# Optimization experiments

Measured on AMD Instinct MI355X. Metric: run time of the kernel, lower is better.

The kernel has to match this reference:

```python
import jax, jax.numpy as jnp
import numpy as np

V = 78864; E = 300; H = 512; A = 300; T = 20; DEC_EMB = 512; START = 2


def _pos_encoding(n, d):
    pos = np.arange(n)[:, None].astype(np.float32)
    i = np.arange(d)[None, :]
    angle = pos / np.power(10000.0, (2 * (i // 2)).astype(np.float32) / d)
    pe = np.where(i % 2 == 0, np.sin(angle), np.cos(angle)).astype(np.float32)
    return jnp.asarray(pe)  # [n, d]


def _lstm_cell(x, h, c, Wih, Whh, b):
    g = x @ Wih.T + h @ Whh.T + b
    i, f, gg, o = jnp.split(g, 4, axis=-1)
    c = jax.nn.sigmoid(f) * c + jax.nn.sigmoid(i) * jnp.tanh(gg)
    h = jax.nn.sigmoid(o) * jnp.tanh(c)
    return h, c


def setup_inputs() -> dict:
    key = jax.random.key(0)
    ks = iter(jax.random.split(key, 48))
    B, L = 40, 1000
    def w(shape, s=0.02):
        return jax.random.normal(next(ks), shape, jnp.float32) * s
    def z(shape):
        return jnp.zeros(shape, jnp.float32)
    inp = dict(
        enc_in=jax.random.randint(next(ks), (B, L), 0, V),
        enc_out=jax.random.normal(next(ks), (B, L, H), jnp.float32),
        enc_mask=jnp.zeros((B, L), bool),
        inputs=jax.random.randint(next(ks), (B, T), 0, V),
        embed=w((V, E)),
        elmo1_Wih=w((4 * H, E)), elmo1_Whh=w((4 * H, H)), elmo1_b=z((4 * H,)),
        elmo2_Wih=w((4 * H, H)), elmo2_Whh=w((4 * H, H)), elmo2_b=z((4 * H,)),
        in_W=w((DEC_EMB, H + E + A + H)), in_b=z((DEC_EMB,)),
        rnn1_Wih=w((4 * H, DEC_EMB)), rnn1_Whh=w((4 * H, H)), rnn1_b=z((4 * H,)),
        att1_Wq=w((A, H)), att1_bq=z((A,)), att1_Wk=w((A, H)), att1_bk=z((A,)), att1_Wv=w((A, H)), att1_bv=z((A,)),
        rnn2_Wih=w((4 * H, A)), rnn2_Whh=w((4 * H, H)), rnn2_b=z((4 * H,)),
        att2_Wq=w((A, H)), att2_bq=z((A,)), att2_Wk=w((A, H)), att2_bk=z((A,)), att2_Wv=w((A, H)), att2_bv=z((A,)),
        copy_W=w((A, H)), copy_b=z((A,)),
        out_W=w((V, A)), out_b=z((V,)),
        scale=jnp.asarray(1.0, jnp.float32),
    )
    return inp


def _forward(enc_in, enc_out, enc_mask, inputs, embed,
             elmo1_Wih, elmo1_Whh, elmo1_b, elmo2_Wih, elmo2_Whh, elmo2_b,
             in_W, in_b, rnn1_Wih, rnn1_Whh, rnn1_b,
             att1_Wq, att1_bq, att1_Wk, att1_bk, att1_Wv, att1_bv,
             rnn2_Wih, rnn2_Whh, rnn2_b,
             att2_Wq, att2_bq, att2_Wk, att2_bk, att2_Wv, att2_bv,
             copy_W, copy_b, out_W, out_b, scale):
    B, L = enc_in.shape
    pe = _pos_encoding(T, DEC_EMB)  # [T, 512]
    # Precompute per-encoder projections (hoisted out of the step loop).
    K1 = jnp.einsum('blh,ah->bla', enc_out, att1_Wk) + att1_bk
    V1 = jnp.einsum('blh,ah->bla', enc_out, att1_Wv) + att1_bv
    K2 = jnp.einsum('blh,ah->bla', enc_out, att2_Wk) + att2_bk
    V2 = jnp.einsum('blh,ah->bla', enc_out, att2_Wv) + att2_bv
    copyK = jnp.tanh(jnp.einsum('blh,ah->bla', enc_out, copy_W) + copy_b)
    bidx = jnp.arange(B)[:, None]

    def attn(h, Wq, bq, K, Vp):
        q = h @ Wq.T + bq                          # [B, A]
        s = jnp.einsum('ba,bla->bl', q, K)
        s = jnp.where(enc_mask, -1e9, s)
        p = jax.nn.softmax(s, axis=-1)
        return jnp.einsum('bl,bla->ba', p, Vp)

    # teacher forcing with random_int=0 -> always use ground-truth inputs
    sym_in = jnp.concatenate([jnp.full((B, 1), START, inputs.dtype), inputs[:, :-1]], axis=1).T  # [T,B]
    sym_out = inputs.T  # [T,B]

    zf = lambda *s: jnp.zeros(s, enc_out.dtype)
    carry0 = (zf(B, H), zf(B, H), zf(B, H), zf(B, H),  # elmo h1,c1,h2,c2
              zf(B, H), zf(B, H), zf(B, H), zf(B, H),  # rnn1 h,c ; rnn2 h,c
              zf(B, A), zf(B, H))                       # dec_att_out, select_read

    def step(carry, xs):
        eh1, ec1, eh2, ec2, h1, c1, h2, c2, att, sel = carry
        pe_t, s_in, s_out = xs
        emb = embed[s_in]                                           # [B, E]
        eh1, ec1 = _lstm_cell(emb, eh1, ec1, elmo1_Wih, elmo1_Whh, elmo1_b)
        eh2, ec2 = _lstm_cell(eh1, eh2, ec2, elmo2_Wih, elmo2_Whh, elmo2_b)
        in_embed = jnp.concatenate([emb, eh2], axis=-1)              # [B, 812]
        dec_in = jnp.concatenate([in_embed, att, sel], axis=-1) @ in_W.T + in_b + pe_t
        h1, c1 = _lstm_cell(dec_in, h1, c1, rnn1_Wih, rnn1_Whh, rnn1_b)
        att = attn(h1, att1_Wq, att1_bq, K1, V1)
        h2, c2 = _lstm_cell(att, h2, c2, rnn2_Wih, rnn2_Whh, rnn2_b)
        att = attn(h2, att2_Wq, att2_bq, K2, V2) + att
        # copy scores
        s = jnp.einsum('ba,bla->bl', att, copyK)
        s = jnp.where(enc_mask, -1e9, s)
        score_c = jax.nn.softmax(s, axis=-1)
        score_e = score_c * scale * scale
        vocab = att @ out_W.T + out_b                                # [B, V]
        vocab = vocab.at[bidx, enc_in].add(score_e)
        sym_pred = jnp.argmax(vocab, axis=-1).astype(jnp.int32)
        eq = (enc_in == s_out[:, None]).astype(score_c.dtype)
        score_f = score_c * eq
        score_f = score_f / (jnp.sum(score_f, axis=-1, keepdims=True) + 1e-8)
        sel = jnp.einsum('bl,blh->bh', score_f, enc_out)
        return (eh1, ec1, eh2, ec2, h1, c1, h2, c2, att, sel), (vocab, sym_pred)

    _, (dec_out, syms) = jax.lax.scan(step, carry0, (pe, sym_in, sym_out))
    return jnp.transpose(dec_out, (1, 0, 2)), syms.T  # [B,T,V], [B,T]


def reference(enc_in, enc_out, enc_mask, inputs, embed,
              elmo1_Wih, elmo1_Whh, elmo1_b, elmo2_Wih, elmo2_Whh, elmo2_b,
              in_W, in_b, rnn1_Wih, rnn1_Whh, rnn1_b,
              att1_Wq, att1_bq, att1_Wk, att1_bk, att1_Wv, att1_bv,
              rnn2_Wih, rnn2_Whh, rnn2_b,
              att2_Wq, att2_bq, att2_Wk, att2_bk, att2_Wv, att2_bv,
              copy_W, copy_b, out_W, out_b, scale):
    return _forward(enc_in, enc_out, enc_mask, inputs, embed,
                    elmo1_Wih, elmo1_Whh, elmo1_b, elmo2_Wih, elmo2_Whh, elmo2_b,
                    in_W, in_b, rnn1_Wih, rnn1_Whh, rnn1_b,
                    att1_Wq, att1_bq, att1_Wk, att1_bk, att1_Wv, att1_bv,
                    rnn2_Wih, rnn2_Whh, rnn2_b,
                    att2_Wq, att2_bq, att2_Wk, att2_bk, att2_Wv, att2_bv,
                    copy_W, copy_b, out_W, out_b, scale)
```

## Files before the change

kernel.cpp:

```cpp
#include <hip/hip_runtime.h>
#include <math.h>

#define B_ 40
#define L_ 1000
#define H_ 512
#define A_ 300
#define T_ 20
#define E_ 300
#define V_ 78864
#define START_ 2

#define NBLK 256
#define NTHR 512
#define NVT 309

#define OFF_CKH   0ul
#define OFF_M1T   6400000ul
#define OFF_M2T   6662144ul
#define OFF_BQK1  6924288ul
#define OFF_BQK2  6924800ul
#define OFF_QK    6925312ul
#define OFF_DEC   6945792ul
#define OFF_ATT1  6966272ul
#define OFF_CPART 6978272ul
#define OFF_CSTAT 7101152ul
#define OFF_ATTA  7101632ul
#define OFF_SCCA  7341632ul
#define OFF_STT   8141632ul
#define OFF_ATT2  8469312ul
#define OFF_SELP  8481312ul
#define OFF_FLAGS 8604192ul
#define OFF_REL   8612384ul
#define WS_END    8612448ul

struct P {
  const int* enc_in; const float* enc; const unsigned char* mask; const int* inputs;
  const float* embed;
  const float *e1Wih,*e1Whh,*e1b,*e2Wih,*e2Whh,*e2b;
  const float *inW,*inb;
  const float *r1Wih,*r1Whh,*r1b;
  const float *a1Wq,*a1bq,*a1Wk,*a1Wv,*a1bv;
  const float *r2Wih,*r2Whh,*r2b;
  const float *a2Wq,*a2bq,*a2Wk,*a2Wv,*a2bv;
  const float *cW,*cb,*oW,*ob,*scale;
  float* dout;
  unsigned short* copyKh;
  float *M1T,*M2T,*bqk1,*bqk2,*qk,*dec,*att1,*cpart,*cstat,*attTall,*sccAll,*stt,*att2,*selp;
  unsigned *flags,*rel;
};

__device__ __forceinline__ float sigm(float x){ return 1.0f/(1.0f+expf(-x)); }

__device__ __forceinline__ float wredSum(float v){
#pragma unroll
  for(int o=32;o>0;o>>=1) v+=__shfl_xor(v,o);
  return v;
}
__device__ __forceinline__ float wredMax(float v){
#pragma unroll
  for(int o=32;o>0;o>>=1) v=fmaxf(v,__shfl_xor(v,o));
  return v;
}
__device__ __forceinline__ unsigned short f2bf(float f){
  unsigned u=__float_as_uint(f);
  u=(u+0x7fffu+((u>>16)&1u))>>16;
  return (unsigned short)u;
}

__device__ __forceinline__ void gbar2(unsigned* flags, unsigned* rel, unsigned epoch){
  __syncthreads();
  int tid=threadIdx.x;
  if(blockIdx.x==0){
    if(tid>0 && tid<NBLK){
      while(__hip_atomic_load(flags+(unsigned)tid*32u,__ATOMIC_RELAXED,__HIP_MEMORY_SCOPE_AGENT)<epoch)
        __builtin_amdgcn_s_sleep(2);
      (void)__hip_atomic_load(flags+(unsigned)tid*32u,__ATOMIC_ACQUIRE,__HIP_MEMORY_SCOPE_AGENT);
    }
    __syncthreads();
    if(tid==0)
      __hip_atomic_store(rel,epoch,__ATOMIC_RELEASE,__HIP_MEMORY_SCOPE_AGENT);
  } else {
    if(tid==0){
      __hip_atomic_store(flags+(unsigned)blockIdx.x*32u,epoch,__ATOMIC_RELEASE,__HIP_MEMORY_SCOPE_AGENT);
      while(__hip_atomic_load(rel,__ATOMIC_RELAXED,__HIP_MEMORY_SCOPE_AGENT)<epoch)
        __builtin_amdgcn_s_sleep(2);
      (void)__hip_atomic_load(rel,__ATOMIC_ACQUIRE,__HIP_MEMORY_SCOPE_AGENT);
    }
    __syncthreads();
  }
}

template<typename SRC>
static __device__ __forceinline__ void gv_accum(float* xs,int K,const float* Wrow,
    float& acc,int lane,int kq,int nq,SRC src){
  for(int k0=0;k0<K;k0+=256){
    int ch=min(256,K-k0);
    __syncthreads();
    if(ch==256){
      float r[20];
#pragma unroll
      for(int u=0;u<20;u++){
        int i=threadIdx.x+u*NTHR;
        r[u]=src(i>>8,k0+(i&255));
      }
#pragma unroll
      for(int u=0;u<20;u++){
        int i=threadIdx.x+u*NTHR;
        xs[(i>>8)*257+(i&255)]=r[u];
      }
    } else {
      for(int i=threadIdx.x;i<40*ch;i+=NTHR){
        int bb=i/ch, kk=i-bb*ch;
        xs[bb*257+kk]=src(bb,k0+kk);
      }
    }
    __syncthreads();
    if(lane<40){
      float a0=0.f,a1=0.f,a2=0.f,a3=0.f;
      int k=kq;
      for(;k+3*nq<ch;k+=4*nq){
        a0+=Wrow[k0+k     ]*xs[lane*257+k];
        a1+=Wrow[k0+k+  nq]*xs[lane*257+k+  nq];
        a2+=Wrow[k0+k+2*nq]*xs[lane*257+k+2*nq];
        a3+=Wrow[k0+k+3*nq]*xs[lane*257+k+3*nq];
      }
      for(;k<ch;k+=nq) a0+=Wrow[k0+k]*xs[lane*257+k];
      acc+=a0+a1+a2+a3;
    }
  }
}

static __device__ void lstm_ph(const P& p,float* SH,float* gld,int t,
    const float* Wih,int XD,const float* Whh,const float* bias,
    const float* xvec,bool gather,
    const float* hr,const float* cr,float* hw,float* cw){
  int tid=threadIdx.x,w=tid>>6,lane=tid&63;
  int gate=w&3,usub=w>>2;
  int row=gate*H_+(blockIdx.x*2+usub);
  int rowu=__builtin_amdgcn_readfirstlane(row);
  float acc=bias[rowu];
  const float* W1=Wih+(size_t)rowu*XD;
  if(gather){
    const int* inp=p.inputs; const float* emb=p.embed; int tt=t;
    gv_accum(SH,XD,W1,acc,lane,0,1,[=](int bb,int kk)->float{
      int si=(tt==0)?START_:inp[bb*T_+tt-1];
      return emb[(size_t)si*E_+kk];});
  }else{
    gv_accum(SH,XD,W1,acc,lane,0,1,[=](int bb,int kk)->float{
      return xvec[(size_t)bb*XD+kk];});
  }
  const float* W2=Whh+(size_t)rowu*H_;
  gv_accum(SH,H_,W2,acc,lane,0,1,[=](int bb,int kk)->float{
    return hr[bb*H_+kk];});
  gld[w*64+lane]=acc;
  __syncthreads();
  if(w<2&&lane<40){
    int u=blockIdx.x*2+w,b=lane;
    float gi=gld[(w*4+0)*64+b],gf=gld[(w*4+1)*64+b],gg=gld[(w*4+2)*64+b],go=gld[(w*4+3)*64+b];
    float c=cr[b*H_+u];
    float cn=sigm(gf)*c+sigm(gi)*tanhf(gg);
    hw[b*H_+u]=sigm(go)*tanhf(cn);
    cw[b*H_+u]=cn;
  }
  __syncthreads();
}

static __device__ void qk_ph(const P& p,float* SH,const float* hsrc,
    const float* MT,const float* bqk){
  int tid=threadIdx.x;
  if(blockIdx.x>=240) return;
  int b=blockIdx.x/6, j=blockIdx.x%6;
  SH[tid]=hsrc[b*H_+tid];
  __syncthreads();
  int h0=j*86, hc=min(86,H_-h0);
  if(tid<hc){
    int hp=h0+tid;
    float a=bqk[hp];
    const float4* mr=(const float4*)(MT+(size_t)hp*H_);
#pragma unroll 8
    for(int i=0;i<H_/4;i++){
      float4 m4=mr[i];
      a+=SH[4*i]*m4.x+SH[4*i+1]*m4.y+SH[4*i+2]*m4.z+SH[4*i+3]*m4.w;
    }
    p.qk[b*H_+hp]=a;
  }
}

static __device__ void scctx_ph(const P& p,float* SH){
  int tid=threadIdx.x,w=tid>>6,lane=tid&63;
  if(blockIdx.x>=240) return;
  int b=blockIdx.x/6, j=blockIdx.x%6;
  int l0=j*167, lcnt=min(167,L_-l0);
  const float* qrow=p.qk+b*H_;
  float4 q0=*(const float4*)(qrow+lane*8);
  float4 q1=*(const float4*)(qrow+lane*8+4);
  float* tile=SH;
  float* sc24=SH+12288;
  const float4* base=(const float4*)(p.enc+((size_t)(b*L_+l0))*H_);
  float4 pre[6];
  { int rem=lcnt*128;
#pragma unroll
    for(int u=0;u<6;u++){ int i=tid+u*NTHR; pre[u]=(i<rem)?base[i]:make_float4(0.f,0.f,0.f,0.f); } }
  float m=-3.0e38f,S=0.f,acc=0.f;
  for(int t0=0;t0<lcnt;t0+=24){
    int tc=min(24,lcnt-t0);
    __syncthreads();
    { float4* dst=(float4*)tile;
#pragma unroll
      for(int u=0;u<6;u++){ int i=tid+u*NTHR; if(i<tc*128) dst[i]=pre[u]; } }
    __syncthreads();
    if(t0+24<lcnt){
      int rem=(lcnt-t0-24)*128;
      const float4* src=base+(size_t)(t0+24)*128;
#pragma unroll
      for(int u=0;u<6;u++){ int i=tid+u*NTHR; pre[u]=(i<rem)?src[i]:make_float4(0.f,0.f,0.f,0.f); }
    }
#pragma unroll
    for(int r=0;r<3;r++){
      int row=w*3+r;
      float sc=-1e30f;
      if(row<tc){
        const float4* er=(const float4*)(tile+row*512);
        float4 e0=er[lane*2], e1=er[lane*2+1];
        float pp=q0.x*e0.x+q0.y*e0.y+q0.z*e0.z+q0.w*e0.w
                +q1.x*e1.x+q1.y*e1.y+q1.z*e1.z+q1.w*e1.w;
        pp=wredSum(pp);
        sc=p.mask[b*L_+l0+t0+row]?-1e9f:pp;
      }
      if(lane==0) sc24[row]=sc;
    }
    __syncthreads();
    float tm=-3.0e38f;
    for(int r=0;r<tc;r++) tm=fmaxf(tm,sc24[r]);
    float mn=fmaxf(m,tm);
    float scl=expf(m-mn);
    float Sadd=0.f, aadd=0.f;
    for(int r=0;r<tc;r++){
      float pe=expf(sc24[r]-mn);
      Sadd+=pe;
      aadd+=pe*tile[r*512+tid];
    }
    S=S*scl+Sadd;
    acc=acc*scl+aadd;
    m=mn;
  }
  p.cpart[(size_t)(b*6+j)*H_+tid]=acc;
  if(tid==0){p.cstat[(b*6+j)*2]=m; p.cstat[(b*6+j)*2+1]=S;}
}

static __device__ void atto_ph(const P& p,float* SH,const float* Wv,const float* bv,
    bool ADD,int t){
  int tid=threadIdx.x;
  if(blockIdx.x>=40) return;
  int b=blockIdx.x;
  float mb=-3.0e38f;
#pragma unroll
  for(int j=0;j<6;j++) mb=fmaxf(mb,p.cstat[(b*6+j)*2]);
  float Sb=0.f;
#pragma unroll
  for(int j=0;j<6;j++) Sb+=p.cstat[(b*6+j)*2+1]*expf(p.cstat[(b*6+j)*2]-mb);
  float inv=1.0f/Sb;
  float cx=0.f;
#pragma unroll
  for(int j=0;j<6;j++) cx+=expf(p.cstat[(b*6+j)*2]-mb)*p.cpart[(size_t)(b*6+j)*H_+tid];
  SH[tid]=cx*inv;
  __syncthreads();
  if(tid<A_){
    float a=bv[tid];
    const float4* wr=(const float4*)(Wv+(size_t)tid*H_);
#pragma unroll 8
    for(int i=0;i<H_/4;i++){
      float4 w4=wr[i];
      a+=SH[4*i]*w4.x+SH[4*i+1]*w4.y+SH[4*i+2]*w4.z+SH[4*i+3]*w4.w;
    }
    if(ADD){
      a+=p.att1[b*A_+tid];
      p.att2[b*A_+tid]=a;
      p.attTall[(size_t)t*A_*B_+tid*B_+b]=a;
    }
    else p.att1[b*A_+tid]=a;
  }
}

static __device__ void copysc_ph(const P& p,int t){
  int tid=threadIdx.x,w=tid>>6,lane=tid&63;
  if(blockIdx.x>=240) return;
  int b=blockIdx.x/6, j=blockIdx.x%6;
  int l0=j*167, lcnt=min(167,L_-l0);
  float* scct=p.sccAll+(size_t)t*B_*L_;
  float ar[8];
#pragma unroll
  for(int q=0;q<8;q++){
    int a=lane*8+q;
    ar[q]=(lane<40&&a<A_)? p.att2[b*A_+a] : 0.f;
  }
  for(int l=l0+w;l<l0+lcnt;l+=8){
    float pp=0.f;
    if(lane<40){
      const uint4* cr=(const uint4*)(p.copyKh+((size_t)(b*L_+l))*320);
      uint4 kk=cr[lane];
      pp =ar[0]*__uint_as_float(kk.x<<16)+ar[1]*__uint_as_float(kk.x&0xffff0000u);
      pp+=ar[2]*__uint_as_float(kk.y<<16)+ar[3]*__uint_as_float(kk.y&0xffff0000u);
      pp+=ar[4]*__uint_as_float(kk.z<<16)+ar[5]*__uint_as_float(kk.z&0xffff0000u);
      pp+=ar[6]*__uint_as_float(kk.w<<16)+ar[7]*__uint_as_float(kk.w&0xffff0000u);
    }
    pp=wredSum(pp);
    if(lane==0) scct[b*L_+l]=p.mask[b*L_+l]?-1e9f:pp;
  }
}

static __device__ void sel_ph(const P& p,float* SH,float* red,int t){
  int tid=threadIdx.x,w=tid>>6,lane=tid&63;
  if(blockIdx.x>=240) return;
  int b=blockIdx.x/6, j=blockIdx.x%6;
  int l0=j*167, lcnt=min(167,L_-l0);
  const float* scct=p.sccAll+(size_t)t*B_*L_;
  for(int i=tid;i<L_;i+=NTHR) SH[i]=scct[b*L_+i];
  __syncthreads();
  float lm=-3.0e38f;
  for(int i=tid;i<L_;i+=NTHR) lm=fmaxf(lm,SH[i]);
  lm=wredMax(lm);
  if(lane==0) red[w]=lm;
  __syncthreads();
  float m=red[0];
#pragma unroll
  for(int q=1;q<8;q++) m=fmaxf(m,red[q]);
  __syncthreads();
  int so=p.inputs[b*T_+t];
  float ls=0.f,lq=0.f;
  for(int i=tid;i<L_;i+=NTHR){
    float exv=expf(SH[i]-m);
    ls+=exv;
    if(p.enc_in[b*L_+i]==so) lq+=exv;
  }
  ls=wredSum(ls); lq=wredSum(lq);
  if(lane==0){red[w]=ls; red[8+w]=lq;}
  __syncthreads();
  float S=0.f,Q=0.f;
#pragma unroll
  for(int q=0;q<8;q++){S+=red[q];Q+=red[8+q];}
  if(tid<lcnt){
    int l=l0+tid;
    float exv=expf(SH[l]-m);
    SH[1024+tid]=(p.enc_in[b*L_+l]==so)?exv:0.f;
  }
  __syncthreads();
  int h4=tid&127, rg=tid>>7;
  float4 a4=make_float4(0.f,0.f,0.f,0.f);
#pragma unroll 2
  for(int li=rg;li<lcnt;li+=4){
    float wgt=SH[1024+li];
    float4 ev=*(const float4*)(p.enc+((size_t)(b*L_+l0+li))*H_+h4*4);
    a4.x+=wgt*ev.x; a4.y+=wgt*ev.y; a4.z+=wgt*ev.z; a4.w+=wgt*ev.w;
  }
  *(float4*)(SH+2048+tid*4)=a4;
  __syncthreads();
  float inv=1.0f/(Q+1e-8f*S);
  float s=SH[2048+tid]+SH[2048+512+tid]+SH[2048+1024+tid]+SH[2048+1536+tid];
  p.selp[(size_t)(b*6+j)*H_+tid]=s*inv;
}

__global__ __launch_bounds__(NTHR,2) void k_persist(P p){
  __shared__ float SH[12544];
  __shared__ float gld[512];
  __shared__ float red[16];
  int blk=blockIdx.x, tid=threadIdx.x;
  unsigned bt=0;
#define BARR() do{bt++; gbar2(p.flags,p.rel,bt);}while(0)

  {
    int mm=blk>>7, r0=(blk&127)*4;
    const float* Wq = mm? p.a2Wq : p.a1Wq;
    const float* Wk = mm? p.a2Wk : p.a1Wk;
    float* MT = mm? p.M2T : p.M1T;
    float s0=0.f,s1=0.f,s2=0.f,s3=0.f;
    for(int a=0;a<A_;a++){
      float wq=Wq[a*H_+tid];
      s0+=wq*Wk[a*H_+r0+0];
      s1+=wq*Wk[a*H_+r0+1];
      s2+=wq*Wk[a*H_+r0+2];
      s3+=wq*Wk[a*H_+r0+3];
    }
    MT[(size_t)(r0+0)*H_+tid]=s0;
    MT[(size_t)(r0+1)*H_+tid]=s1;
    MT[(size_t)(r0+2)*H_+tid]=s2;
    MT[(size_t)(r0+3)*H_+tid]=s3;
    if((blk&127)==0){
      const float* bq = mm? p.a2bq : p.a1bq;
      float ab=0.f;
      for(int a=0;a<A_;a++) ab+=bq[a]*Wk[a*H_+tid];
      (mm? p.bqk2 : p.bqk1)[tid]=ab;
    }
  }
  for(int item=blk;item<B_*63;item+=NBLK){
    int b=item/63, lt=item-b*63;
    int l0=lt*16, lcnt=min(16,L_-l0);
    float acc[16];
    float bv=(tid<A_)?p.cb[tid]:0.f;
#pragma unroll
    for(int l=0;l<16;l++) acc[l]=bv;
    for(int k0=0;k0<H_;k0+=32){
      __syncthreads();
      for(int i=tid;i<A_*32;i+=NTHR){
        int a=i>>5,kc=i&31;
        SH[a*33+kc]=p.cW[(size_t)a*H_+k0+kc];
      }
      __syncthreads();
      if(tid<A_){
#pragma unroll
        for(int l=0;l<16;l++){
          if(l<lcnt){
            const float* es=p.enc+((size_t)(b*L_+l0+l))*H_+k0;
            float al=acc[l];
#pragma unroll
            for(int kc=0;kc<32;kc++) al+=SH[tid*33+kc]*es[kc];
            acc[l]=al;
          }
        }
      }
    }
    if(tid<320){
#pragma unroll
      for(int l=0;l<16;l++){
        if(l<lcnt){
          unsigned short hv=0;
          if(tid<A_) hv=f2bf(tanhf(acc[l]));
          p.copyKh[((size_t)(b*L_+l0+l))*320+tid]=hv;
        }
      }
    }
  }
  BARR();

  for(int t=0;t<T_;t++){
    int rp=t&1, wp=rp^1;
    float* stt=p.stt;
    auto SL=[&](int i,int par){ return stt+((size_t)(i*2+par))*(B_*H_); };
    float *eh1r=SL(0,rp),*eh1w=SL(0,wp),*ec1r=SL(1,rp),*ec1w=SL(1,wp);
    float *eh2r=SL(2,rp),*eh2w=SL(2,wp),*ec2r=SL(3,rp),*ec2w=SL(3,wp);
    float *h1r=SL(4,rp),*h1w=SL(4,wp),*c1r=SL(5,rp),*c1w=SL(5,wp);
    float *h2r=SL(6,rp),*h2w=SL(6,wp),*c2r=SL(7,rp),*c2w=SL(7,wp);

    lstm_ph(p,SH,gld,t,p.e1Wih,E_,p.e1Whh,p.e1b,nullptr,true ,eh1r,ec1r,eh1w,ec1w); BARR();
    lstm_ph(p,SH,gld,t,p.e2Wih,H_,p.e2Whh,p.e2b,eh1w  ,false,eh2r,ec2r,eh2w,ec2w); BARR();

    {
      int w=tid>>6,lane=tid&63;
      int usub=w>>2, kq=w&3;
      int unit=blk*2+usub;
      int rowu=__builtin_amdgcn_readfirstlane(unit);
      float acc=0.f;
      const float* Wr=p.inW+(size_t)rowu*1624;
      const int* inp=p.inputs; const float* emb=p.embed;
      const float* e2=eh2w; const float* a2c=p.att2; const float* sp=p.selp;
      int tt=t;
      gv_accum(SH,1624,Wr,acc,lane,kq,4,[=](int bb,int kk)->float{
        if(kk<E_){int si=(tt==0)?START_:inp[bb*T_+tt-1];return emb[(size_t)si*E_+kk];}
        else if(kk<E_+H_) return e2[bb*H_+kk-E_];
        else if(kk<E_+H_+A_) return a2c[bb*A_+kk-(E_+H_)];
        else{
          int hh=kk-(E_+H_+A_); float s=0.f;
#pragma unroll
          for(int jj=0;jj<6;jj++) s+=sp[(size_t)(bb*6+jj)*H_+hh];
          return s;
        }
      });
      gld[(usub*4+kq)*64+lane]=acc;
      __syncthreads();
      if(w<2&&lane<40){
        int u=blk*2+w;
        float s=gld[(w*4+0)*64+lane]+gld[(w*4+1)*64+lane]
               +gld[(w*4+2)*64+lane]+gld[(w*4+3)*64+lane];
        float ex=(float)(2*(u>>1))/512.0f;
        float ang=(float)t/powf(10000.0f,ex);
        s+=p.inb[u]+((u&1)?cosf(ang):sinf(ang));
        p.dec[lane*H_+u]=s;
      }
      __syncthreads();
    }
    BARR();

    lstm_ph(p,SH,gld,t,p.r1Wih,H_,p.r1Whh,p.r1b,p.dec ,false,h1r,c1r,h1w,c1w); BARR();
    qk_ph(p,SH,h1w,p.M1T,p.bqk1);                                              BARR();
    scctx_ph(p,SH);                                                            BARR();
    atto_ph(p,SH,p.a1Wv,p.a1bv,false,t);                                       BARR();
    lstm_ph(p,SH,gld,t,p.r2Wih,A_,p.r2Whh,p.r2b,p.att1,false,h2r,c2r,h2w,c2w); BARR();
    qk_ph(p,SH,h2w,p.M2T,p.bqk2);                                              BARR();
    scctx_ph(p,SH);                                                            BARR();
    atto_ph(p,SH,p.a2Wv,p.a2bv,true,t);                                        BARR();
    copysc_ph(p,t);                                                            BARR();
    sel_ph(p,SH,red,t);                                                        BARR();
  }

  {
    int row=tid>>1, half=tid&1;
    for(int item=blk;item<NVT*T_;item+=NBLK){
      int vt=item/T_, t=item-vt*T_;
      long v0=(long)vt*256;
      int vcnt=min(256,(int)(V_-v0));
      float acc[20];
#pragma unroll
      for(int q=0;q<20;q++) acc[q]=0.f;
      for(int c=0;c<10;c++){
        int a0=c*32, aw=min(32,A_-a0);
        __syncthreads();
        if(c<9){
          int tot=vcnt*8;
          for(int i=tid;i<tot;i+=NTHR){
            int vr=i>>3, f=i&7;
            *(float4*)&SH[vr*36+f*4]=*(const float4*)(p.oW+(size_t)(v0+vr)*A_+a0+f*4);
          }
          for(int i=tid;i<32*40;i+=NTHR) SH[9216+i]=p.attTall[(size_t)t*A_*B_+a0*B_+i];
        } else {
          int tot=vcnt*3;
          for(int i=tid;i<tot;i+=NTHR){
            int vr=i/3, f=i-vr*3;
            *(float4*)&SH[vr*36+f*4]=*(const float4*)(p.oW+(size_t)(v0+vr)*A_+a0+f*4);
          }
          for(int i=tid;i<12*40;i+=NTHR) SH[9216+i]=p.attTall[(size_t)t*A_*B_+a0*B_+i];
        }
        __syncthreads();
        if(row<vcnt){
          const float* wrow=&SH[row*36];
          for(int ac=0;ac<aw;ac++){
            float wv=wrow[ac];
            const float* at=&SH[9216+ac*40+half*20];
#pragma unroll
            for(int bq=0;bq<5;bq++){
              float4 t4=*(const float4*)(at+bq*4);
              acc[bq*4+0]+=wv*t4.x; acc[bq*4+1]+=wv*t4.y;
              acc[bq*4+2]+=wv*t4.z; acc[bq*4+3]+=wv*t4.w;
            }
          }
        }
      }
      if(row<vcnt){
        long v=v0+row;
        float obv=p.ob[v];
#pragma unroll
        for(int bb=0;bb<20;bb++){
          int b=half*20+bb;
          p.dout[((size_t)(b*T_+t))*V_+v]=acc[bb]+obv;
        }
      }
    }
  }
  BARR();

  {
    int w=tid>>6,lane=tid&63;
    float sc2=p.scale[0]*p.scale[0];
    for(int it=blk;it<B_*T_;it+=NBLK){
      int b=it/T_, t=it-b*T_;
      const float* scr=p.sccAll+((size_t)t*B_+b)*L_;
      __syncthreads();
      for(int i=tid;i<L_;i+=NTHR) SH[i]=scr[i];
      __syncthreads();
      float lm=-3.0e38f;
      for(int i=tid;i<L_;i+=NTHR) lm=fmaxf(lm,SH[i]);
      lm=wredMax(lm);
      if(lane==0) red[w]=lm;
      __syncthreads();
      float m=red[0];
#pragma unroll
      for(int q=1;q<8;q++) m=fmaxf(m,red[q]);
      __syncthreads();
      float ls=0.f;
      for(int i=tid;i<L_;i+=NTHR) ls+=expf(SH[i]-m);
      ls=wredSum(ls);
      if(lane==0) red[w]=ls;
      __syncthreads();
      float S=0.f;
#pragma unroll
      for(int q=0;q<8;q++) S+=red[q];
      float f=sc2/S;
      float* drow=p.dout+((size_t)(b*T_+t))*V_;
      const int* ei=p.enc_in+b*L_;
      for(int i=tid;i<L_;i+=NTHR) atomicAdd(drow+ei[i], expf(SH[i]-m)*f);
      __syncthreads();
    }
  }
  BARR();

  {
    int* isa=(int*)(SH+512);
    for(int it=blk;it<B_*T_;it+=NBLK){
      int b=it/T_, t=it-b*T_;
      const float* row=p.dout+((size_t)(b*T_+t))*V_;
      float best=-3.0e38f; int bi=0;
      for(int i4=tid;i4<V_/4;i4+=NTHR){
        float4 x=((const float4*)row)[i4];
        int base=i4*4;
        if(x.x>best){best=x.x;bi=base;}
        if(x.y>best){best=x.y;bi=base+1;}
        if(x.z>best){best=x.z;bi=base+2;}
        if(x.w>best){best=x.w;bi=base+3;}
      }
      __syncthreads();
      SH[tid]=best; isa[tid]=bi;
      __syncthreads();
      for(int off=256;off>0;off>>=1){
        if(tid<off){
          float ov=SH[tid+off]; int oi=isa[tid+off];
          if(ov>SH[tid]||(ov==SH[tid]&&oi<isa[tid])){SH[tid]=ov; isa[tid]=oi;}
        }
        __syncthreads();
      }
      if(tid==0) p.dout[(size_t)B_*T_*V_+b*T_+t]=(float)isa[0];
    }
  }
#undef BARR
}

extern "C" void kernel_launch(void* const* d_in, const int* in_sizes, int n_in,
                              void* d_out, int out_size, void* d_ws, size_t ws_size,
                              hipStream_t stream){
  P p;
  p.enc_in=(const int*)d_in[0];
  p.enc   =(const float*)d_in[1];
  p.mask  =(const unsigned char*)d_in[2];
  p.inputs=(const int*)d_in[3];
  p.embed =(const float*)d_in[4];
  p.e1Wih=(const float*)d_in[5];  p.e1Whh=(const float*)d_in[6];  p.e1b=(const float*)d_in[7];
  p.e2Wih=(const float*)d_in[8];  p.e2Whh=(const float*)d_in[9];  p.e2b=(const float*)d_in[10];
  p.inW  =(const float*)d_in[11]; p.inb  =(const float*)d_in[12];
  p.r1Wih=(const float*)d_in[13]; p.r1Whh=(const float*)d_in[14]; p.r1b=(const float*)d_in[15];
  p.a1Wq =(const float*)d_in[16]; p.a1bq =(const float*)d_in[17];
  p.a1Wk =(const float*)d_in[18];
  p.a1Wv =(const float*)d_in[20]; p.a1bv =(const float*)d_in[21];
  p.r2Wih=(const float*)d_in[22]; p.r2Whh=(const float*)d_in[23]; p.r2b=(const float*)d_in[24];
  p.a2Wq =(const float*)d_in[25]; p.a2bq =(const float*)d_in[26];
  p.a2Wk =(const float*)d_in[27];
  p.a2Wv =(const float*)d_in[29]; p.a2bv =(const float*)d_in[30];
  p.cW   =(const float*)d_in[31]; p.cb   =(const float*)d_in[32];
  p.oW   =(const float*)d_in[33]; p.ob   =(const float*)d_in[34];
  p.scale=(const float*)d_in[35];
  p.dout=(float*)d_out;

  float* w=(float*)d_ws;
  p.copyKh=(unsigned short*)(w+OFF_CKH);
  p.M1T  =w+OFF_M1T;    p.M2T =w+OFF_M2T;
  p.bqk1 =w+OFF_BQK1;   p.bqk2=w+OFF_BQK2;
  p.qk   =w+OFF_QK;     p.dec =w+OFF_DEC;
  p.att1 =w+OFF_ATT1;
  p.cpart=w+OFF_CPART;  p.cstat=w+OFF_CSTAT;
  p.attTall=w+OFF_ATTA; p.sccAll=w+OFF_SCCA;
  p.stt  =w+OFF_STT;
  p.att2 =w+OFF_ATT2;   p.selp=w+OFF_SELP;
  p.flags=(unsigned*)(w+OFF_FLAGS);
  p.rel  =(unsigned*)(w+OFF_REL);

  hipMemsetAsync(w+OFF_STT,0,(WS_END-OFF_STT)*sizeof(float),stream);
  k_persist<<<NBLK,NTHR,0,stream>>>(p);
}
```

Before: 16.09 ms.

## Split persistent kernel into recurrence, vocab, scatter, argmax kernels with 1024 threads

```diff
diff --git a/kernel.cpp b/kernel.cpp
--- a/kernel.cpp
+++ b/kernel.cpp
@@ -11,7 +11,7 @@
 #define START_ 2
 
 #define NBLK 256
-#define NTHR 512
+#define NTHR 1024
 #define NVT 309
 
 #define OFF_CKH   0ul
@@ -29,9 +29,10 @@
 #define OFF_STT   8141632ul
 #define OFF_ATT2  8469312ul
 #define OFF_SELP  8481312ul
-#define OFF_FLAGS 8604192ul
-#define OFF_REL   8612384ul
-#define WS_END    8612448ul
+#define OFF_SELST 8604192ul
+#define OFF_FLAGS 8604912ul
+#define OFF_REL   8613104ul
+#define WS_END    8613168ul
 
 struct P {
   const int* enc_in; const float* enc; const unsigned char* mask; const int* inputs;
@@ -45,7 +46,7 @@
   const float *cW,*cb,*oW,*ob,*scale;
   float* dout;
   unsigned short* copyKh;
-  float *M1T,*M2T,*bqk1,*bqk2,*qk,*dec,*att1,*cpart,*cstat,*attTall,*sccAll,*stt,*att2,*selp;
+  float *M1T,*M2T,*bqk1,*bqk2,*qk,*dec,*att1,*cpart,*cstat,*attTall,*sccAll,*stt,*att2,*selp,*selstat;
   unsigned *flags,*rel;
 };
 
@@ -73,7 +74,7 @@
   if(blockIdx.x==0){
     if(tid>0 && tid<NBLK){
       while(__hip_atomic_load(flags+(unsigned)tid*32u,__ATOMIC_RELAXED,__HIP_MEMORY_SCOPE_AGENT)<epoch)
-        __builtin_amdgcn_s_sleep(2);
+        __builtin_amdgcn_s_sleep(8);
       (void)__hip_atomic_load(flags+(unsigned)tid*32u,__ATOMIC_ACQUIRE,__HIP_MEMORY_SCOPE_AGENT);
     }
     __syncthreads();
@@ -83,7 +84,7 @@
     if(tid==0){
       __hip_atomic_store(flags+(unsigned)blockIdx.x*32u,epoch,__ATOMIC_RELEASE,__HIP_MEMORY_SCOPE_AGENT);
       while(__hip_atomic_load(rel,__ATOMIC_RELAXED,__HIP_MEMORY_SCOPE_AGENT)<epoch)
-        __builtin_amdgcn_s_sleep(2);
+        __builtin_amdgcn_s_sleep(8);
       (void)__hip_atomic_load(rel,__ATOMIC_ACQUIRE,__HIP_MEMORY_SCOPE_AGENT);
     }
     __syncthreads();
@@ -97,17 +98,11 @@
     int ch=min(256,K-k0);
     __syncthreads();
     if(ch==256){
-      float r[20];
-#pragma unroll
-      for(int u=0;u<20;u++){
-        int i=threadIdx.x+u*NTHR;
-        r[u]=src(i>>8,k0+(i&255));
-      }
-#pragma unroll
-      for(int u=0;u<20;u++){
-        int i=threadIdx.x+u*NTHR;
-        xs[(i>>8)*257+(i&255)]=r[u];
-      }
+      float r[10];
+#pragma unroll
+      for(int u=0;u<10;u++){ int i=threadIdx.x+u*NTHR; r[u]=src(i>>8,k0+(i&255)); }
+#pragma unroll
+      for(int u=0;u<10;u++){ int i=threadIdx.x+u*NTHR; xs[(i>>8)*257+(i&255)]=r[u]; }
     } else {
       for(int i=threadIdx.x;i<40*ch;i+=NTHR){
         int bb=i/ch, kk=i-bb*ch;
@@ -135,31 +130,34 @@
     const float* xvec,bool gather,
     const float* hr,const float* cr,float* hw,float* cw){
   int tid=threadIdx.x,w=tid>>6,lane=tid&63;
-  int gate=w&3,usub=w>>2;
+  int gate=w&3,ks=(w>>2)&1,usub=w>>3;
   int row=gate*H_+(blockIdx.x*2+usub);
   int rowu=__builtin_amdgcn_readfirstlane(row);
-  float acc=bias[rowu];
+  float acc=0.f;
   const float* W1=Wih+(size_t)rowu*XD;
   if(gather){
     const int* inp=p.inputs; const float* emb=p.embed; int tt=t;
-    gv_accum(SH,XD,W1,acc,lane,0,1,[=](int bb,int kk)->float{
+    gv_accum(SH,XD,W1,acc,lane,ks,2,[=](int bb,int kk)->float{
       int si=(tt==0)?START_:inp[bb*T_+tt-1];
       return emb[(size_t)si*E_+kk];});
   }else{
-    gv_accum(SH,XD,W1,acc,lane,0,1,[=](int bb,int kk)->float{
+    gv_accum(SH,XD,W1,acc,lane,ks,2,[=](int bb,int kk)->float{
       return xvec[(size_t)bb*XD+kk];});
   }
   const float* W2=Whh+(size_t)rowu*H_;
-  gv_accum(SH,H_,W2,acc,lane,0,1,[=](int bb,int kk)->float{
+  gv_accum(SH,H_,W2,acc,lane,ks,2,[=](int bb,int kk)->float{
     return hr[bb*H_+kk];});
   gld[w*64+lane]=acc;
   __syncthreads();
   if(w<2&&lane<40){
     int u=blockIdx.x*2+w,b=lane;
-    float gi=gld[(w*4+0)*64+b],gf=gld[(w*4+1)*64+b],gg=gld[(w*4+2)*64+b],go=gld[(w*4+3)*64+b];
+    float g0=gld[((w<<3)|0)*64+b]+gld[((w<<3)|4)*64+b]+bias[0*H_+u];
+    float g1=gld[((w<<3)|1)*64+b]+gld[((w<<3)|5)*64+b]+bias[1*H_+u];
+    float g2=gld[((w<<3)|2)*64+b]+gld[((w<<3)|6)*64+b]+bias[2*H_+u];
+    float g3=gld[((w<<3)|3)*64+b]+gld[((w<<3)|7)*64+b]+bias[3*H_+u];
     float c=cr[b*H_+u];
-    float cn=sigm(gf)*c+sigm(gi)*tanhf(gg);
-    hw[b*H_+u]=sigm(go)*tanhf(cn);
+    float cn=sigm(g1)*c+sigm(g0)*tanhf(g2);
+    hw[b*H_+u]=sigm(g3)*tanhf(cn);
     cw[b*H_+u]=cn;
   }
   __syncthreads();
@@ -170,19 +168,22 @@
   int tid=threadIdx.x;
   if(blockIdx.x>=240) return;
   int b=blockIdx.x/6, j=blockIdx.x%6;
-  SH[tid]=hsrc[b*H_+tid];
-  __syncthreads();
+  if(tid<512) SH[tid]=hsrc[b*H_+tid];
+  __syncthreads();
+  int rp2=tid>>1, hf=tid&1;
   int h0=j*86, hc=min(86,H_-h0);
-  if(tid<hc){
-    int hp=h0+tid;
-    float a=bqk[hp];
-    const float4* mr=(const float4*)(MT+(size_t)hp*H_);
-#pragma unroll 8
-    for(int i=0;i<H_/4;i++){
-      float4 m4=mr[i];
-      a+=SH[4*i]*m4.x+SH[4*i+1]*m4.y+SH[4*i+2]*m4.z+SH[4*i+3]*m4.w;
-    }
-    p.qk[b*H_+hp]=a;
+  if(rp2<hc){
+    int hp=h0+rp2;
+    const float4* mr=(const float4*)(MT+(size_t)hp*H_)+hf*64;
+    const float4* hs=((const float4*)SH)+hf*64;
+    float a=0.f;
+#pragma unroll 16
+    for(int i=0;i<64;i++){
+      float4 m4=mr[i],h4=hs[i];
+      a+=m4.x*h4.x+m4.y*h4.y+m4.z*h4.z+m4.w*h4.w;
+    }
+    a+=__shfl_xor(a,1);
+    if(hf==0) p.qk[b*H_+hp]=a+bqk[hp];
   }
 }
 
@@ -195,29 +196,30 @@
   float4 q0=*(const float4*)(qrow+lane*8);
   float4 q1=*(const float4*)(qrow+lane*8+4);
   float* tile=SH;
-  float* sc24=SH+12288;
+  float* sc32=SH+16384;
   const float4* base=(const float4*)(p.enc+((size_t)(b*L_+l0))*H_);
-  float4 pre[6];
+  float4 pre[4];
   { int rem=lcnt*128;
 #pragma unroll
-    for(int u=0;u<6;u++){ int i=tid+u*NTHR; pre[u]=(i<rem)?base[i]:make_float4(0.f,0.f,0.f,0.f); } }
+    for(int u=0;u<4;u++){ int i=tid+u*NTHR; pre[u]=(i<rem)?base[i]:make_float4(0.f,0.f,0.f,0.f); } }
+  int h=tid>>1, rh=tid&1;
   float m=-3.0e38f,S=0.f,acc=0.f;
-  for(int t0=0;t0<lcnt;t0+=24){
-    int tc=min(24,lcnt-t0);
+  for(int t0=0;t0<lcnt;t0+=32){
+    int tc=min(32,lcnt-t0);
     __syncthreads();
     { float4* dst=(float4*)tile;
 #pragma unroll
-      for(int u=0;u<6;u++){ int i=tid+u*NTHR; if(i<tc*128) dst[i]=pre[u]; } }
-    __syncthreads();
-    if(t0+24<lcnt){
-      int rem=(lcnt-t0-24)*128;
-      const float4* src=base+(size_t)(t0+24)*128;
-#pragma unroll
-      for(int u=0;u<6;u++){ int i=tid+u*NTHR; pre[u]=(i<rem)?src[i]:make_float4(0.f,0.f,0.f,0.f); }
-    }
-#pragma unroll
-    for(int r=0;r<3;r++){
-      int row=w*3+r;
+      for(int u=0;u<4;u++){ int i=tid+u*NTHR; if(i<tc*128) dst[i]=pre[u]; } }
+    __syncthreads();
+    if(t0+32<lcnt){
+      int rem=(lcnt-t0-32)*128;
+      const float4* src=base+(size_t)(t0+32)*128;
+#pragma unroll
+      for(int u=0;u<4;u++){ int i=tid+u*NTHR; pre[u]=(i<rem)?src[i]:make_float4(0.f,0.f,0.f,0.f); }
+    }
+#pragma unroll
+    for(int r=0;r<2;r++){
+      int row=w*2+r;
       float sc=-1e30f;
       if(row<tc){
         const float4* er=(const float4*)(tile+row*512);
@@ -227,24 +229,26 @@
         pp=wredSum(pp);
         sc=p.mask[b*L_+l0+t0+row]?-1e9f:pp;
       }
-      if(lane==0) sc24[row]=sc;
+      if(lane==0) sc32[row]=sc;
     }
     __syncthreads();
     float tm=-3.0e38f;
-    for(int r=0;r<tc;r++) tm=fmaxf(tm,sc24[r]);
+    for(int r=0;r<tc;r++) tm=fmaxf(tm,sc32[r]);
     float mn=fmaxf(m,tm);
     float scl=expf(m-mn);
-    float Sadd=0.f, aadd=0.f;
-    for(int r=0;r<tc;r++){
-      float pe=expf(sc24[r]-mn);
-      Sadd+=pe;
-      aadd+=pe*tile[r*512+tid];
-    }
-    S=S*scl+Sadd;
-    acc=acc*scl+aadd;
+    float Sa=0.f, aa=0.f;
+    for(int r=rh;r<tc;r+=2){
+      float pe=expf(sc32[r]-mn);
+      Sa+=pe;
+      aa+=pe*tile[r*512+h];
+    }
+    S=S*scl+Sa;
+    acc=acc*scl+aa;
     m=mn;
   }
-  p.cpart[(size_t)(b*6+j)*H_+tid]=acc;
+  S+=__shfl_xor(S,1);
+  acc+=__shfl_xor(acc,1);
+  if(rh==0) p.cpart[(size_t)(b*6+j)*H_+h]=acc;
   if(tid==0){p.cstat[(b*6+j)*2]=m; p.cstat[(b*6+j)*2+1]=S;}
 }
 
@@ -260,41 +264,54 @@
 #pragma unroll
   for(int j=0;j<6;j++) Sb+=p.cstat[(b*6+j)*2+1]*expf(p.cstat[(b*6+j)*2]-mb);
   float inv=1.0f/Sb;
-  float cx=0.f;
-#pragma unroll
-  for(int j=0;j<6;j++) cx+=expf(p.cstat[(b*6+j)*2]-mb)*p.cpart[(size_t)(b*6+j)*H_+tid];
-  SH[tid]=cx*inv;
-  __syncthreads();
-  if(tid<A_){
-    float a=bv[tid];
-    const float4* wr=(const float4*)(Wv+(size_t)tid*H_);
-#pragma unroll 8
-    for(int i=0;i<H_/4;i++){
-      float4 w4=wr[i];
-      a+=SH[4*i]*w4.x+SH[4*i+1]*w4.y+SH[4*i+2]*w4.z+SH[4*i+3]*w4.w;
-    }
-    if(ADD){
-      a+=p.att1[b*A_+tid];
-      p.att2[b*A_+tid]=a;
-      p.attTall[(size_t)t*A_*B_+tid*B_+b]=a;
-    }
-    else p.att1[b*A_+tid]=a;
-  }
-}
-
-static __device__ void copysc_ph(const P& p,int t){
+  if(tid<512){
+    float cx=0.f;
+#pragma unroll
+    for(int j=0;j<6;j++) cx+=expf(p.cstat[(b*6+j)*2]-mb)*p.cpart[(size_t)(b*6+j)*H_+tid];
+    SH[tid]=cx*inv;
+  }
+  __syncthreads();
+  int rp2=tid>>1, hf=tid&1;
+  if(rp2<A_){
+    const float4* wr=(const float4*)(Wv+(size_t)rp2*H_)+hf*64;
+    const float4* cs=((const float4*)SH)+hf*64;
+    float a=0.f;
+#pragma unroll 16
+    for(int i=0;i<64;i++){
+      float4 w4=wr[i],c4=cs[i];
+      a+=w4.x*c4.x+w4.y*c4.y+w4.z*c4.z+w4.w*c4.w;
+    }
+    a+=__shfl_xor(a,1);
+    if(hf==0){
+      a+=bv[rp2];
+      if(ADD){
+        a+=p.att1[b*A_+rp2];
+        p.att2[b*A_+rp2]=a;
+        p.attTall[(size_t)t*A_*B_+rp2*B_+b]=a;
+      } else p.att1[b*A_+rp2]=a;
+    }
+  }
+}
+
+static __device__ void copyscsel_ph(const P& p,float* SH,float* red,int t){
   int tid=threadIdx.x,w=tid>>6,lane=tid&63;
   if(blockIdx.x>=240) return;
   int b=blockIdx.x/6, j=blockIdx.x%6;
   int l0=j*167, lcnt=min(167,L_-l0);
   float* scct=p.sccAll+(size_t)t*B_*L_;
+  float* sccL=SH;
+  float* sccE=SH+176;
+  int* nzc=(int*)(SH+352);
+  int* nzl=(int*)(SH+356);
+  if(tid==0) *nzc=0;
   float ar[8];
 #pragma unroll
   for(int q=0;q<8;q++){
     int a=lane*8+q;
     ar[q]=(lane<40&&a<A_)? p.att2[b*A_+a] : 0.f;
   }
-  for(int l=l0+w;l<l0+lcnt;l+=8){
+  float mw=-3.0e38f;
+  for(int l=l0+w;l<l0+lcnt;l+=16){
     float pp=0.f;
     if(lane<40){
       const uint4* cr=(const uint4*)(p.copyKh+((size_t)(b*L_+l))*320);
@@ -305,70 +322,56 @@
       pp+=ar[6]*__uint_as_float(kk.w<<16)+ar[7]*__uint_as_float(kk.w&0xffff0000u);
     }
     pp=wredSum(pp);
-    if(lane==0) scct[b*L_+l]=p.mask[b*L_+l]?-1e9f:pp;
-  }
-}
-
-static __device__ void sel_ph(const P& p,float* SH,float* red,int t){
-  int tid=threadIdx.x,w=tid>>6,lane=tid&63;
-  if(blockIdx.x>=240) return;
-  int b=blockIdx.x/6, j=blockIdx.x%6;
-  int l0=j*167, lcnt=min(167,L_-l0);
-  const float* scct=p.sccAll+(size_t)t*B_*L_;
-  for(int i=tid;i<L_;i+=NTHR) SH[i]=scct[b*L_+i];
-  __syncthreads();
-  float lm=-3.0e38f;
-  for(int i=tid;i<L_;i+=NTHR) lm=fmaxf(lm,SH[i]);
-  lm=wredMax(lm);
-  if(lane==0) red[w]=lm;
+    float v=p.mask[b*L_+l]?-1e9f:pp;
+    if(lane==0){ scct[b*L_+l]=v; sccL[l-l0]=v; }
+    mw=fmaxf(mw,v);
+  }
+  if(lane==0) red[w]=mw;
   __syncthreads();
   float m=red[0];
 #pragma unroll
-  for(int q=1;q<8;q++) m=fmaxf(m,red[q]);
+  for(int q=1;q<16;q++) m=fmaxf(m,red[q]);
   __syncthreads();
   int so=p.inputs[b*T_+t];
-  float ls=0.f,lq=0.f;
-  for(int i=tid;i<L_;i+=NTHR){
-    float exv=expf(SH[i]-m);
-    ls+=exv;
-    if(p.enc_in[b*L_+i]==so) lq+=exv;
-  }
-  ls=wredSum(ls); lq=wredSum(lq);
-  if(lane==0){red[w]=ls; red[8+w]=lq;}
+  float e=0.f,qe=0.f;
+  if(tid<lcnt){
+    e=expf(sccL[tid]-m);
+    bool eq=(p.enc_in[b*L_+l0+tid]==so);
+    sccE[tid]=eq?e:0.f;
+    if(eq){ int k=atomicAdd(nzc,1); nzl[k]=tid; qe=e; }
+  }
+  float ls=wredSum(e), lq=wredSum(qe);
+  if(lane==0){ red[w]=ls; red[16+w]=lq; }
   __syncthreads();
   float S=0.f,Q=0.f;
 #pragma unroll
-  for(int q=0;q<8;q++){S+=red[q];Q+=red[8+q];}
-  if(tid<lcnt){
-    int l=l0+tid;
-    float exv=expf(SH[l]-m);
-    SH[1024+tid]=(p.enc_in[b*L_+l]==so)?exv:0.f;
-  }
-  __syncthreads();
-  int h4=tid&127, rg=tid>>7;
-  float4 a4=make_float4(0.f,0.f,0.f,0.f);
-#pragma unroll 2
-  for(int li=rg;li<lcnt;li+=4){
-    float wgt=SH[1024+li];
-    float4 ev=*(const float4*)(p.enc+((size_t)(b*L_+l0+li))*H_+h4*4);
-    a4.x+=wgt*ev.x; a4.y+=wgt*ev.y; a4.z+=wgt*ev.z; a4.w+=wgt*ev.w;
-  }
-  *(float4*)(SH+2048+tid*4)=a4;
-  __syncthreads();
-  float inv=1.0f/(Q+1e-8f*S);
-  float s=SH[2048+tid]+SH[2048+512+tid]+SH[2048+1024+tid]+SH[2048+1536+tid];
-  p.selp[(size_t)(b*6+j)*H_+tid]=s*inv;
-}
-
-__global__ __launch_bounds__(NTHR,2) void k_persist(P p){
-  __shared__ float SH[12544];
-  __shared__ float gld[512];
-  __shared__ float red[16];
+  for(int q=0;q<16;q++){S+=red[q];Q+=red[16+q];}
+  int nz=*nzc;
+  if(tid<512){
+    float pp=0.f;
+    for(int k=0;k<nz;k++){
+      int row=nzl[k];
+      pp+=sccE[row]*p.enc[((size_t)(b*L_+l0+row))*H_+tid];
+    }
+    p.selp[(size_t)(b*6+j)*H_+tid]=pp;
+  }
+  if(tid==0){
+    p.selstat[(size_t)(b*6+j)*3+0]=m;
+    p.selstat[(size_t)(b*6+j)*3+1]=S;
+    p.selstat[(size_t)(b*6+j)*3+2]=Q;
+  }
+}
+
+__global__ __launch_bounds__(NTHR) void k_rec(P p){
+  __shared__ float SH[16448];
+  __shared__ float gld[1024];
+  __shared__ float red[32];
+  __shared__ float ssc[240];
   int blk=blockIdx.x, tid=threadIdx.x;
   unsigned bt=0;
 #define BARR() do{bt++; gbar2(p.flags,p.rel,bt);}while(0)
 
-  {
+  if(tid<512){
     int mm=blk>>7, r0=(blk&127)*4;
     const float* Wq = mm? p.a2Wq : p.a1Wq;
     const float* Wk = mm? p.a2Wk : p.a1Wk;
@@ -445,32 +448,52 @@
     lstm_ph(p,SH,gld,t,p.e2Wih,H_,p.e2Whh,p.e2b,eh1w  ,false,eh2r,ec2r,eh2w,ec2w); BARR();
 
     {
+      if(tid<40){
+        float mj[6],Sj[6],Qj[6];
+#pragma unroll
+        for(int jj=0;jj<6;jj++){
+          mj[jj]=p.selstat[(size_t)(tid*6+jj)*3+0];
+          Sj[jj]=p.selstat[(size_t)(tid*6+jj)*3+1];
+          Qj[jj]=p.selstat[(size_t)(tid*6+jj)*3+2];
+        }
+        float ms=mj[0];
+#pragma unroll
+        for(int jj=1;jj<6;jj++) ms=fmaxf(ms,mj[jj]);
+        float Ss=0.f,Qs=0.f;
+#pragma unroll
+        for(int jj=0;jj<6;jj++){ float ee=expf(mj[jj]-ms); Ss+=ee*Sj[jj]; Qs+=ee*Qj[jj]; }
+        float inv=(Ss>0.f)?1.0f/(Qs+1e-8f*Ss):0.f;
+#pragma unroll
+        for(int jj=0;jj<6;jj++) ssc[tid*6+jj]=expf(mj[jj]-ms)*inv;
+      }
       int w=tid>>6,lane=tid&63;
-      int usub=w>>2, kq=w&3;
+      int usub=w>>3, kq=w&7;
       int unit=blk*2+usub;
       int rowu=__builtin_amdgcn_readfirstlane(unit);
       float acc=0.f;
       const float* Wr=p.inW+(size_t)rowu*1624;
       const int* inp=p.inputs; const float* emb=p.embed;
       const float* e2=eh2w; const float* a2c=p.att2; const float* sp=p.selp;
+      float* sscl=ssc;
       int tt=t;
-      gv_accum(SH,1624,Wr,acc,lane,kq,4,[=](int bb,int kk)->float{
+      gv_accum(SH,1624,Wr,acc,lane,kq,8,[=](int bb,int kk)->float{
         if(kk<E_){int si=(tt==0)?START_:inp[bb*T_+tt-1];return emb[(size_t)si*E_+kk];}
         else if(kk<E_+H_) return e2[bb*H_+kk-E_];
         else if(kk<E_+H_+A_) return a2c[bb*A_+kk-(E_+H_)];
         else{
           int hh=kk-(E_+H_+A_); float s=0.f;
 #pragma unroll
-          for(int jj=0;jj<6;jj++) s+=sp[(size_t)(bb*6+jj)*H_+hh];
+          for(int jj=0;jj<6;jj++) s+=sscl[bb*6+jj]*sp[(size_t)(bb*6+jj)*H_+hh];
           return s;
         }
       });
-      gld[(usub*4+kq)*64+lane]=acc;
+      gld[((usub<<3)|kq)*64+lane]=acc;
       __syncthreads();
       if(w<2&&lane<40){
         int u=blk*2+w;
-        float s=gld[(w*4+0)*64+lane]+gld[(w*4+1)*64+lane]
-               +gld[(w*4+2)*64+lane]+gld[(w*4+3)*64+lane];
+        float s=0.f;
+#pragma unroll
+        for(int q=0;q<8;q++) s+=gld[((w<<3)|q)*64+lane];
         float ex=(float)(2*(u>>1))/512.0f;
         float ang=(float)t/powf(10000.0f,ex);
         s+=p.inb[u]+((u&1)?cosf(ang):sinf(ang));
@@ -488,128 +511,111 @@
     qk_ph(p,SH,h2w,p.M2T,p.bqk2);                                              BARR();
     scctx_ph(p,SH);                                                            BARR();
     atto_ph(p,SH,p.a2Wv,p.a2bv,true,t);                                        BARR();
-    copysc_ph(p,t);                                                            BARR();
-    sel_ph(p,SH,red,t);                                                        BARR();
-  }
-
-  {
-    int row=tid>>1, half=tid&1;
-    for(int item=blk;item<NVT*T_;item+=NBLK){
-      int vt=item/T_, t=item-vt*T_;
-      long v0=(long)vt*256;
-      int vcnt=min(256,(int)(V_-v0));
-      float acc[20];
-#pragma unroll
-      for(int q=0;q<20;q++) acc[q]=0.f;
-      for(int c=0;c<10;c++){
-        int a0=c*32, aw=min(32,A_-a0);
-        __syncthreads();
-        if(c<9){
-          int tot=vcnt*8;
-          for(int i=tid;i<tot;i+=NTHR){
-            int vr=i>>3, f=i&7;
-            *(float4*)&SH[vr*36+f*4]=*(const float4*)(p.oW+(size_t)(v0+vr)*A_+a0+f*4);
-          }
-          for(int i=tid;i<32*40;i+=NTHR) SH[9216+i]=p.attTall[(size_t)t*A_*B_+a0*B_+i];
-        } else {
-          int tot=vcnt*3;
-          for(int i=tid;i<tot;i+=NTHR){
-            int vr=i/3, f=i-vr*3;
-            *(float4*)&SH[vr*36+f*4]=*(const float4*)(p.oW+(size_t)(v0+vr)*A_+a0+f*4);
-          }
-          for(int i=tid;i<12*40;i+=NTHR) SH[9216+i]=p.attTall[(size_t)t*A_*B_+a0*B_+i];
+    copyscsel_ph(p,SH,red,t);                                                  BARR();
+  }
+#undef BARR
+}
+
+__global__ __launch_bounds__(NTHR) void k_vocab(P p){
+  __shared__ float SH[10496];
+  int tid=threadIdx.x;
+  int item=blockIdx.x;
+  int vt=item/T_, t=item-vt*T_;
+  long v0=(long)vt*256;
+  if(v0>=V_) return;
+  int vcnt=min(256,(int)(V_-v0));
+  int row=tid>>2, qtr=tid&3;
+  float acc[10];
+#pragma unroll
+  for(int q=0;q<10;q++) acc[q]=0.f;
+  for(int c=0;c<10;c++){
+    int a0=c*32, aw=min(32,A_-a0);
+    int awf4=aw>>2;
+    __syncthreads();
+    for(int i=tid;i<vcnt*awf4;i+=NTHR){
+      int vr=i/awf4, f=i-vr*awf4;
+      *(float4*)&SH[vr*36+f*4]=*(const float4*)(p.oW+(size_t)(v0+vr)*A_+a0+f*4);
+    }
+    for(int i=tid;i<aw*40;i+=NTHR) SH[9216+i]=p.attTall[(size_t)t*A_*B_+a0*B_+i];
+    __syncthreads();
+    if(row<vcnt){
+      const float* wrow=&SH[row*36];
+      for(int ac=0;ac<aw;ac++){
+        float wv=wrow[ac];
+        const float2* at=(const float2*)&SH[9216+ac*40+qtr*10];
+#pragma unroll
+        for(int bq=0;bq<5;bq++){
+          float2 t2=at[bq];
+          acc[bq*2+0]+=wv*t2.x;
+          acc[bq*2+1]+=wv*t2.y;
         }
-        __syncthreads();
-        if(row<vcnt){
-          const float* wrow=&SH[row*36];
-          for(int ac=0;ac<aw;ac++){
-            float wv=wrow[ac];
-            const float* at=&SH[9216+ac*40+half*20];
-#pragma unroll
-            for(int bq=0;bq<5;bq++){
-              float4 t4=*(const float4*)(at+bq*4);
-              acc[bq*4+0]+=wv*t4.x; acc[bq*4+1]+=wv*t4.y;
-              acc[bq*4+2]+=wv*t4.z; acc[bq*4+3]+=wv*t4.w;
-            }
-          }
-        }
-      }
-      if(row<vcnt){
-        long v=v0+row;
-        float obv=p.ob[v];
-#pragma unroll
-        for(int bb=0;bb<20;bb++){
-          int b=half*20+bb;
-          p.dout[((size_t)(b*T_+t))*V_+v]=acc[bb]+obv;
-        }
-      }
-    }
-  }
-  BARR();
-
-  {
-    int w=tid>>6,lane=tid&63;
-    float sc2=p.scale[0]*p.scale[0];
-    for(int it=blk;it<B_*T_;it+=NBLK){
-      int b=it/T_, t=it-b*T_;
-      const float* scr=p.sccAll+((size_t)t*B_+b)*L_;
-      __syncthreads();
-      for(int i=tid;i<L_;i+=NTHR) SH[i]=scr[i];
-      __syncthreads();
-      float lm=-3.0e38f;
-      for(int i=tid;i<L_;i+=NTHR) lm=fmaxf(lm,SH[i]);
-      lm=wredMax(lm);
-      if(lane==0) red[w]=lm;
-      __syncthreads();
-      float m=red[0];
-#pragma unroll
-      for(int q=1;q<8;q++) m=fmaxf(m,red[q]);
-      __syncthreads();
-      float ls=0.f;
-      for(int i=tid;i<L_;i+=NTHR) ls+=expf(SH[i]-m);
-      ls=wredSum(ls);
-      if(lane==0) red[w]=ls;
-      __syncthreads();
-      float S=0.f;
-#pragma unroll
-      for(int q=0;q<8;q++) S+=red[q];
-      float f=sc2/S;
-      float* drow=p.dout+((size_t)(b*T_+t))*V_;
-      const int* ei=p.enc_in+b*L_;
-      for(int i=tid;i<L_;i+=NTHR) atomicAdd(drow+ei[i], expf(SH[i]-m)*f);
-      __syncthreads();
-    }
-  }
-  BARR();
-
-  {
-    int* isa=(int*)(SH+512);
-    for(int it=blk;it<B_*T_;it+=NBLK){
-      int b=it/T_, t=it-b*T_;
-      const float* row=p.dout+((size_t)(b*T_+t))*V_;
-      float best=-3.0e38f; int bi=0;
-      for(int i4=tid;i4<V_/4;i4+=NTHR){
-        float4 x=((const float4*)row)[i4];
-        int base=i4*4;
-        if(x.x>best){best=x.x;bi=base;}
-        if(x.y>best){best=x.y;bi=base+1;}
-        if(x.z>best){best=x.z;bi=base+2;}
-        if(x.w>best){best=x.w;bi=base+3;}
-      }
-      __syncthreads();
-      SH[tid]=best; isa[tid]=bi;
-      __syncthreads();
-      for(int off=256;off>0;off>>=1){
-        if(tid<off){
-          float ov=SH[tid+off]; int oi=isa[tid+off];
-          if(ov>SH[tid]||(ov==SH[tid]&&oi<isa[tid])){SH[tid]=ov; isa[tid]=oi;}
-        }
-        __syncthreads();
-      }
-      if(tid==0) p.dout[(size_t)B_*T_*V_+b*T_+t]=(float)isa[0];
-    }
-  }
-#undef BARR
+      }
+    }
+  }
+  if(row<vcnt){
+    long v=v0+row;
+    float obv=p.ob[v];
+#pragma unroll
+    for(int bb=0;bb<10;bb++){
+      int b=qtr*10+bb;
+      p.dout[((size_t)(b*T_+t))*V_+v]=acc[bb]+obv;
+    }
+  }
+}
+
+__global__ __launch_bounds__(NTHR) void k_scatter(P p){
+  __shared__ float SH[1000];
+  __shared__ float red[16];
+  int tid=threadIdx.x,w=tid>>6,lane=tid&63;
+  int b=blockIdx.x/T_, t=blockIdx.x%T_;
+  const float* scr=p.sccAll+((size_t)t*B_+b)*L_;
+  if(tid<L_) SH[tid]=scr[tid];
+  __syncthreads();
+  float lm=(tid<L_)?SH[tid]:-3.0e38f;
+  lm=wredMax(lm);
+  if(lane==0) red[w]=lm;
+  __syncthreads();
+  float m=red[0];
+#pragma unroll
+  for(int q=1;q<16;q++) m=fmaxf(m,red[q]);
+  __syncthreads();
+  float e=(tid<L_)?expf(SH[tid]-m):0.f;
+  float ls=wredSum(e);
+  if(lane==0) red[w]=ls;
+  __syncthreads();
+  float S=0.f;
+#pragma unroll
+  for(int q=0;q<16;q++) S+=red[q];
+  float f=p.scale[0]*p.scale[0]/S;
+  if(tid<L_)
+    atomicAdd(p.dout+((size_t)(b*T_+t))*V_+p.enc_in[b*L_+tid], e*f);
+}
+
+__global__ __launch_bounds__(NTHR) void k_argmax(P p){
+  __shared__ float vs[1024];
+  __shared__ int isa[1024];
+  int tid=threadIdx.x;
+  int b=blockIdx.x/T_, t=blockIdx.x%T_;
+  const float* row=p.dout+((size_t)(b*T_+t))*V_;
+  float best=-3.0e38f; int bi=0;
+  for(int i4=tid;i4<V_/4;i4+=NTHR){
+    float4 x=((const float4*)row)[i4];
+    int base=i4*4;
+    if(x.x>best){best=x.x;bi=base;}
+    if(x.y>best){best=x.y;bi=base+1;}
+    if(x.z>best){best=x.z;bi=base+2;}
+    if(x.w>best){best=x.w;bi=base+3;}
+  }
+  vs[tid]=best; isa[tid]=bi;
+  __syncthreads();
+  for(int off=512;off>0;off>>=1){
+    if(tid<off){
+      float ov=vs[tid+off]; int oi=isa[tid+off];
+      if(ov>vs[tid]||(ov==vs[tid]&&oi<isa[tid])){vs[tid]=ov; isa[tid]=oi;}
+    }
+    __syncthreads();
+  }
+  if(tid==0) p.dout[(size_t)B_*T_*V_+b*T_+t]=(float)isa[0];
 }
 
 extern "C" void kernel_launch(void* const* d_in, const int* in_sizes, int n_in,
@@ -647,9 +653,13 @@
   p.attTall=w+OFF_ATTA; p.sccAll=w+OFF_SCCA;
   p.stt  =w+OFF_STT;
   p.att2 =w+OFF_ATT2;   p.selp=w+OFF_SELP;
+  p.selstat=w+OFF_SELST;
   p.flags=(unsigned*)(w+OFF_FLAGS);
   p.rel  =(unsigned*)(w+OFF_REL);
 
   hipMemsetAsync(w+OFF_STT,0,(WS_END-OFF_STT)*sizeof(float),stream);
-  k_persist<<<NBLK,NTHR,0,stream>>>(p);
-}
+  k_rec<<<NBLK,NTHR,0,stream>>>(p);
+  k_vocab<<<NVT*T_,NTHR,0,stream>>>(p);
+  k_scatter<<<B_*T_,NTHR,0,stream>>>(p);
+  k_argmax<<<B_*T_,NTHR,0,stream>>>(p);
+}
```

After: 15.61 ms. -3.0%, faster.
